# Kernel tuning notes

Measured on AMD Instinct MI355X. Metric: run time of the kernel, lower is better.

The kernel has to match this reference:

```python
import jax, jax.numpy as jnp
import numpy as np

B, S, D, H, F = 2, 2048, 1024, 16, 4096
DK = D // H
EPS = 1e-6


def _ln(x, g, b):
    mu = jnp.mean(x, axis=-1, keepdims=True)
    var = jnp.mean(jnp.square(x - mu), axis=-1, keepdims=True)
    return (x - mu) * jax.lax.rsqrt(var + EPS) * g + b


def setup_inputs() -> dict:
    key = jax.random.key(0)
    ks = jax.random.split(key, 8)
    sc = 0.02
    return {
        "x": jax.random.normal(ks[0], (B, S, D), jnp.float32),
        "wq": jax.random.normal(ks[1], (D, D), jnp.float32) * sc,
        "bq": jnp.zeros((D,), jnp.float32),
        "wk": jax.random.normal(ks[2], (D, D), jnp.float32) * sc,
        "bk": jnp.zeros((D,), jnp.float32),
        "wv": jax.random.normal(ks[3], (D, D), jnp.float32) * sc,
        "bv": jnp.zeros((D,), jnp.float32),
        "wo": jax.random.normal(ks[4], (D, D), jnp.float32) * sc,
        "bo": jnp.zeros((D,), jnp.float32),
        "w1": jax.random.normal(ks[5], (D, F), jnp.float32) * sc,
        "b1": jnp.zeros((F,), jnp.float32),
        "w2": jax.random.normal(ks[6], (F, D), jnp.float32) * sc,
        "b2": jnp.zeros((D,), jnp.float32),
        "g1": jnp.ones((D,), jnp.float32),
        "be1": jnp.zeros((D,), jnp.float32),
        "g2": jnp.ones((D,), jnp.float32),
        "be2": jnp.zeros((D,), jnp.float32),
    }


def reference(x, wq, bq, wk, bk, wv, bv, wo, bo, w1, b1, w2, b2, g1, be1, g2, be2):
    # Multi-head self-attention (no masks, eval-mode dropout = identity)
    q = (x @ wq + bq).reshape(B, S, H, DK)
    k = (x @ wk + bk).reshape(B, S, H, DK)
    v = (x @ wv + bv).reshape(B, S, H, DK)
    scale = 1.0 / (DK ** 0.5)
    score = jnp.einsum('bihd,bjhd->bhij', q, k) * scale  # [B,H,S,S]
    p = jax.nn.softmax(score, axis=-1)
    attn = jnp.einsum('bhij,bjhd->bihd', p, v).reshape(B, S, D)
    attn = attn @ wo + bo
    # residual + LayerNorm 1
    h = _ln(x + attn, g1, be1)
    # FFN (relu) + residual + LayerNorm 2
    ff = jax.nn.relu(h @ w1 + b1) @ w2 + b2
    return _ln(h + ff, g2, be2)
```

## Files before the change

### kernel.cpp

```cpp
#include <hip/hip_runtime.h>
#include <hip/hip_bf16.h>
#include <cmath>

typedef __bf16 bf16_t;
typedef __bf16 bf16x4 __attribute__((ext_vector_type(4)));
typedef __bf16 bf16x8 __attribute__((ext_vector_type(8)));
typedef float  f32x4  __attribute__((ext_vector_type(4)));

__device__ __forceinline__ void gld_lds16(const bf16_t* g, bf16_t* l) {
    __builtin_amdgcn_global_load_lds(
        (const __attribute__((address_space(1))) void*)g,
        (__attribute__((address_space(3))) void*)l,
        16, 0, 0);
}


struct PrepArgs {
    const float* w[6]; bf16_t* wt[6];
    int K[6], N[6], start[6];
    const float* x; bf16_t* xb; int castStart;
    const float* bq; const float* bk; float* bqkv; int biasStart;
};

__global__ __launch_bounds__(256) void prep(PrepArgs pa) {
    __shared__ float tile[32][33];
    const int bid = blockIdx.x, t = threadIdx.x;
    if (bid < pa.castStart) {
        int mi = 0;
#pragma unroll
        for (int i = 1; i < 6; i++) if (bid >= pa.start[i]) mi = i;
        const int tt  = bid - pa.start[mi];
        const int nbx = pa.N[mi] >> 5;
        const int n0 = (tt % nbx) * 32, k0 = (tt / nbx) * 32;
        const float* in = pa.w[mi];
        bf16_t* out = pa.wt[mi];
        const int K = pa.K[mi], N = pa.N[mi];
        const int tx = t & 31, ty = t >> 5;
#pragma unroll
        for (int i = 0; i < 4; i++) {
            int kk = ty + i * 8;
            tile[kk][tx] = in[(size_t)(k0 + kk) * N + n0 + tx];
        }
        __syncthreads();
#pragma unroll
        for (int i = 0; i < 4; i++) {
            int nn = ty + i * 8;
            out[(size_t)(n0 + nn) * K + k0 + tx] = (bf16_t)tile[tx][nn];
        }
    } else if (bid < pa.biasStart) {
        int i = (bid - pa.castStart) * 256 + t;
        f32x4 v = ((const f32x4*)pa.x)[i];
        bf16x4 o;
        o[0] = (bf16_t)v[0]; o[1] = (bf16_t)v[1]; o[2] = (bf16_t)v[2]; o[3] = (bf16_t)v[3];
        ((bf16x4*)pa.xb)[i] = o;
    } else {
#pragma unroll
        for (int j = 0; j < 8; j++) {
            int idx = t * 8 + j;
            pa.bqkv[idx] = idx < 1024 ? pa.bq[idx] : pa.bk[idx - 1024];
        }
    }
}

__global__ __launch_bounds__(512, 1) void gemm_deep(
    const bf16_t* __restrict__ A, const bf16_t* __restrict__ Bt,
    const float* __restrict__ bias, bf16_t* __restrict__ Cb,
    int N, int lda, int K, int relu, int nbn) {
    __shared__ __attribute__((aligned(16))) bf16_t As[4][256 * 32];
    __shared__ __attribute__((aligned(16))) bf16_t Bs[4][256 * 32];
    const int tid  = threadIdx.x;
    const int lane = tid & 63;
    const int wave = tid >> 6;
    const int wm = wave >> 2, wn = wave & 3;

    const int span  = 8 * nbn;
    const int group = blockIdx.x / span;
    const int rem   = blockIdx.x % span;
    const int bm    = group * 8 + (rem & 7);
    const int bn    = rem >> 3;

    const int srow   = tid >> 2;
    const int slot_s = ((tid & 3) ^ ((tid >> 3) & 3)) * 8;
    const bf16_t* Ag = A  + (size_t)(bm * 256 + srow) * lda + slot_s;
    const bf16_t* Bg = Bt + (size_t)(bn * 256 + srow) * lda + slot_s;

    auto stage = [&](int kk, int buf) {
        gld_lds16(Ag + kk,                       &As[buf][0]        + tid * 8);
        gld_lds16(Ag + (size_t)128 * lda + kk,   &As[buf][128 * 32] + tid * 8);
        gld_lds16(Bg + kk,                       &Bs[buf][0]        + tid * 8);
        gld_lds16(Bg + (size_t)128 * lda + kk,   &Bs[buf][128 * 32] + tid * 8);
    };

    f32x4 acc[8][4] = {};
    const int mrow = lane & 15;
    const int qsw  = (((lane >> 4) ^ ((mrow >> 1) & 3))) * 8;

    auto compute = [&](int cur) {
        bf16x8 bfr[4], af[8];
#pragma unroll
        for (int n = 0; n < 4; n++)
            bfr[n] = *(const bf16x8*)(&Bs[cur][(wn * 64 + n * 16 + mrow) * 32 + qsw]);
#pragma unroll
        for (int mt = 0; mt < 8; mt++)
            af[mt] = *(const bf16x8*)(&As[cur][(wm * 128 + mt * 16 + mrow) * 32 + qsw]);
        __builtin_amdgcn_s_setprio(1);
#pragma unroll
        for (int mt = 0; mt < 8; mt++)
#pragma unroll
            for (int n = 0; n < 4; n++)
                acc[mt][n] = __builtin_amdgcn_mfma_f32_16x16x32_bf16(
                    af[mt], bfr[n], acc[mt][n], 0, 0, 0);
        __builtin_amdgcn_s_setprio(0);
    };

    stage(0, 0); stage(32, 1); stage(64, 2);
    const int nst = K >> 5;
    for (int t = 0; t + 3 < nst; ++t) {
        stage((t + 3) * 32, (t + 3) & 3);
        asm volatile("s_waitcnt vmcnt(12)" ::: "memory");
        __builtin_amdgcn_s_barrier();
        compute(t & 3);
        asm volatile("s_waitcnt lgkmcnt(0)" ::: "memory");
        __builtin_amdgcn_s_barrier();
    }
    asm volatile("s_waitcnt vmcnt(8)" ::: "memory");
    __builtin_amdgcn_s_barrier();
    compute((nst - 3) & 3);
    asm volatile("s_waitcnt lgkmcnt(0)" ::: "memory");
    __builtin_amdgcn_s_barrier();
    asm volatile("s_waitcnt vmcnt(4)" ::: "memory");
    __builtin_amdgcn_s_barrier();
    compute((nst - 2) & 3);
    asm volatile("s_waitcnt lgkmcnt(0)" ::: "memory");
    __builtin_amdgcn_s_barrier();
    asm volatile("s_waitcnt vmcnt(0)" ::: "memory");
    __builtin_amdgcn_s_barrier();
    compute((nst - 1) & 3);

    const int rq = (lane >> 4) * 4;
#pragma unroll
    for (int mt = 0; mt < 8; mt++) {
        int row0 = bm * 256 + wm * 128 + mt * 16 + rq;
#pragma unroll
        for (int n = 0; n < 4; n++) {
            int col = bn * 256 + wn * 64 + n * 16 + mrow;
            float bvc = bias ? bias[col] : 0.f;
#pragma unroll
            for (int r = 0; r < 4; r++) {
                float v = acc[mt][n][r] + bvc;
                if (relu) v = fmaxf(v, 0.f);
                Cb[(size_t)(row0 + r) * N + col] = (bf16_t)v;
            }
        }
    }
}

template<int BN>
__global__ __launch_bounds__(512, 2) void gemm_bt256(
    const bf16_t* __restrict__ A, const bf16_t* __restrict__ Bt,
    const float* __restrict__ bias,
    float* __restrict__ Cf, bf16_t* __restrict__ Cb,
    int M, int N, int lda, int Kloc, int relu, int nbn,
    long bt_bstride, long c_bstride) {
    constexpr int NT = BN / 64;
    constexpr int WN = BN / 4;
    __shared__ __attribute__((aligned(16))) bf16_t As[2][2][256 * 32];
    __shared__ __attribute__((aligned(16))) bf16_t Bs[2][2][BN * 32];
    const int tid  = threadIdx.x;
    const int lane = tid & 63;
    const int wave = tid >> 6;
    const int wm = wave >> 2, wn = wave & 3;
    const int kh = blockIdx.z;

    const int span  = 8 * nbn;
    const int group = blockIdx.x / span;
    const int rem   = blockIdx.x % span;
    const int bm    = group * 8 + (rem & 7);
    const int bn    = rem >> 3;

    const bf16_t* Bt_b = Bt + (size_t)blockIdx.y * bt_bstride;
    float*  Cf_b = Cf ? Cf + (size_t)blockIdx.y * c_bstride + (size_t)kh * M * N : nullptr;
    bf16_t* Cb_b = Cb ? Cb + (size_t)blockIdx.y * c_bstride : nullptr;
    const int koff = kh * Kloc;

    const int r4 = tid >> 2;
    const int kcs = ((tid & 3) ^ ((tid >> 3) & 3)) * 8;
    const bf16_t* Ag = A    + (size_t)(bm * 256 + r4) * lda + koff + kcs;
    const bf16_t* Bg = Bt_b + (size_t)(bn * BN  + r4) * lda + koff + kcs;

    f32x4 acc[8][NT] = {};
    const int mrow = lane & 15;
    const int qsw  = (((lane >> 4) ^ ((mrow >> 1) & 3))) * 8;

    auto stage = [&](int kk, int buf) {
#pragma unroll
        for (int hh = 0; hh < 2; hh++) {
#pragma unroll
            for (int i = 0; i < 2; i++)
                gld_lds16(Ag + (size_t)(i * 128) * lda + kk + hh * 32,
                          &As[buf][hh][i * 128 * 32] + tid * 8);
            if (BN == 256) {
#pragma unroll
                for (int i = 0; i < 2; i++)
                    gld_lds16(Bg + (size_t)(i * 128) * lda + kk + hh * 32,
                              &Bs[buf][hh][i * 128 * 32] + tid * 8);
            } else {
                gld_lds16(Bg + kk + hh * 32, &Bs[buf][hh][0] + tid * 8);
            }
        }
    };

    stage(0, 0);
    __syncthreads();

    const int nsteps = Kloc >> 6;
    for (int st = 0; st < nsteps; ++st) {
        const int cur = st & 1;
        if (st + 1 < nsteps) stage((st + 1) << 6, cur ^ 1);

#pragma unroll
        for (int hh = 0; hh < 2; hh++) {
            bf16x8 bfr[NT];
#pragma unroll
            for (int n = 0; n < NT; n++)
                bfr[n] = *(const bf16x8*)(&Bs[cur][hh][(wn * WN + n * 16 + mrow) * 32 + qsw]);
#pragma unroll
            for (int mt = 0; mt < 8; mt++) {
                bf16x8 af = *(const bf16x8*)(&As[cur][hh][(wm * 128 + mt * 16 + mrow) * 32 + qsw]);
#pragma unroll
                for (int n = 0; n < NT; n++)
                    acc[mt][n] = __builtin_amdgcn_mfma_f32_16x16x32_bf16(
                        af, bfr[n], acc[mt][n], 0, 0, 0);
            }
        }
        __syncthreads();
    }

    const int rq = (lane >> 4) * 4;
#pragma unroll
    for (int mt = 0; mt < 8; mt++) {
        int row0 = bm * 256 + wm * 128 + mt * 16 + rq;
#pragma unroll
        for (int n = 0; n < NT; n++) {
            int col = bn * BN + wn * WN + n * 16 + mrow;
            float bvc = (bias && kh == 0) ? bias[col] : 0.f;
#pragma unroll
            for (int r = 0; r < 4; r++) {
                float v = acc[mt][n][r] + bvc;
                if (relu) v = fmaxf(v, 0.f);
                size_t idx = (size_t)(row0 + r) * N + col;
                if (Cf_b) Cf_b[idx] = v;
                if (Cb_b) Cb_b[idx] = (bf16_t)v;
            }
        }
    }
}

template<int MT>
__global__ __launch_bounds__(256) void gemm_bt(
    const bf16_t* __restrict__ A, const bf16_t* __restrict__ Bt,
    const float* __restrict__ bias,
    float* __restrict__ Cf, bf16_t* __restrict__ Cb,
    int M, int N, int lda, int Kloc, int relu, int nbn, int bias_row,
    long bt_bstride, long c_bstride) {
    constexpr int TM = MT * 32;
    __shared__ __attribute__((aligned(16))) bf16_t As[2][TM * 32];
    __shared__ __attribute__((aligned(16))) bf16_t Bs[2][128 * 32];
    const int tid  = threadIdx.x;
    const int lane = tid & 63;
    const int wave = tid >> 6;
    const int wm = wave & 1, wn = wave >> 1;
    const int kh = blockIdx.z;

    const int span  = 8 * nbn;
    const int group = blockIdx.x / span;
    const int rem   = blockIdx.x % span;
    const int bm    = group * 8 + (rem & 7);
    const int bn    = rem >> 3;

    const bf16_t* Bt_b = Bt + (size_t)blockIdx.y * bt_bstride;
    float*  Cf_b = Cf ? Cf + (size_t)blockIdx.y * c_bstride + (size_t)kh * M * N : nullptr;
    bf16_t* Cb_b = Cb ? Cb + (size_t)blockIdx.y * c_bstride : nullptr;
    const int koff = kh * Kloc;

    const int r4 = tid >> 2;
    const int kcs = ((tid & 3) ^ ((tid >> 3) & 3)) * 8;
    const bf16_t* Ag = A    + (size_t)(bm * TM  + r4) * lda + koff + kcs;
    const bf16_t* Bg = Bt_b + (size_t)(bn * 128 + r4) * lda + koff + kcs;

    f32x4 acc[MT][4] = {};
    const int mrow = lane & 15;
    const int qsw  = (((lane >> 4) ^ ((mrow >> 1) & 3))) * 8;

    auto stage = [&](int kk, int buf) {
#pragma unroll
        for (int i = 0; i < MT / 2; i++)
            gld_lds16(Ag + (size_t)(i * 64) * lda + kk, &As[buf][i * 64 * 32] + tid * 8);
        gld_lds16(Bg + kk,                        &Bs[buf][0] + tid * 8);
        gld_lds16(Bg + (size_t)64 * lda + kk,     &Bs[buf][64 * 32] + tid * 8);
    };

    stage(0, 0);
    __syncthreads();

    const int nt = Kloc >> 5;
    for (int t7 = 0; t7 < nt; ++t7) {
        const int cur = t7 & 1;
        if (t7 + 1 < nt) stage((t7 + 1) << 5, cur ^ 1);

        bf16x8 af[MT], bfr[4];
#pragma unroll
        for (int mt = 0; mt < MT; mt++)
            af[mt] = *(const bf16x8*)(&As[cur][(wm * (MT * 16) + mt * 16 + mrow) * 32 + qsw]);
#pragma unroll
        for (int nt2 = 0; nt2 < 4; nt2++)
            bfr[nt2] = *(const bf16x8*)(&Bs[cur][(wn * 64 + nt2 * 16 + mrow) * 32 + qsw]);
#pragma unroll
        for (int mt = 0; mt < MT; mt++)
#pragma unroll
            for (int nt2 = 0; nt2 < 4; nt2++)
                acc[mt][nt2] = __builtin_amdgcn_mfma_f32_16x16x32_bf16(
                    af[mt], bfr[nt2], acc[mt][nt2], 0, 0, 0);

        __syncthreads();
    }

    const int rq = (lane >> 4) * 4;
#pragma unroll
    for (int mt = 0; mt < MT; mt++) {
        int row0 = bm * TM + wm * (MT * 16) + mt * 16 + rq;
#pragma unroll
        for (int nt2 = 0; nt2 < 4; nt2++) {
            int col = bn * 128 + wn * 64 + nt2 * 16 + mrow;
            float bvc = (bias && kh == 0 && !bias_row) ? bias[col] : 0.f;
#pragma unroll
            for (int r = 0; r < 4; r++) {
                float bb = (bias && kh == 0 && bias_row) ? bias[row0 + r] : bvc;
                float v = acc[mt][nt2][r] + bb;
                if (relu) v = fmaxf(v, 0.f);
                size_t idx = (size_t)(row0 + r) * N + col;
                if (Cf_b) Cf_b[idx] = v;
                if (Cb_b) Cb_b[idx] = (bf16_t)v;
            }
        }
    }
}

__global__ __launch_bounds__(256) void flash_attn_mfma(
    const bf16_t* __restrict__ QKb,
    const bf16_t* __restrict__ Vtg,
    bf16_t* __restrict__ Outb) {
    __shared__ __attribute__((aligned(16))) bf16_t Ks[2][4096];
    __shared__ __attribute__((aligned(16))) bf16_t Vs[2][4096];
    __shared__ __attribute__((aligned(16))) bf16_t Ps[4096];
    const int t = threadIdx.x;
    const int lane = t & 63, wave = t >> 6;
    const int g = lane >> 4, cl = lane & 15;
    const int b = blockIdx.z, h = blockIdx.y, q0 = blockIdx.x * 64;
    const int RS = 2048;
    const bf16_t* Qg = QKb + (size_t)(b * 2048 + q0) * RS + h * 64;
    const bf16_t* Kg = QKb + (size_t)(b * 2048) * RS + 1024 + h * 64;
    const bf16_t* Vg = Vtg + ((size_t)b * 1024 + h * 64) * 2048;

    const int sr  = t >> 2;
    const int scs = (((t & 3) ^ ((t >> 3) & 3))) * 8;

    const bf16_t* Qrow = Qg + (size_t)(wave * 16 + cl) * RS;
    bf16x8 qr0 = *(const bf16x8*)(Qrow + g * 8);
    bf16x8 qr1 = *(const bf16x8*)(Qrow + 32 + g * 8);

    gld_lds16(Kg + (size_t)sr * RS + scs,        &Ks[0][0]    + t * 8);
    gld_lds16(Kg + (size_t)sr * RS + 32 + scs,   &Ks[0][2048] + t * 8);
    gld_lds16(Vg + (size_t)sr * 2048 + scs,      &Vs[0][0]    + t * 8);
    gld_lds16(Vg + (size_t)sr * 2048 + 32 + scs, &Vs[0][2048] + t * 8);
    __syncthreads();

    f32x4 Oacc[4] = {};
    f32x4 Lacc = {};
    bf16x8 ones;
#pragma unroll
    for (int j = 0; j < 8; j++) ones[j] = (bf16_t)1.0f;

    const int rowb = wave * 16 + cl;
    const int psw  = (cl & 7) << 4;
    const int gsw  = ((g ^ ((cl >> 1) & 3))) * 8;
    char* PsB = (char*)Ps;
    const float C = 0.125f * 1.4426950408889634f;

    for (int kt_i = 0; kt_i < 32; ++kt_i) {
        const int cur = kt_i & 1;
        if (kt_i + 1 < 32) {
            const int nb  = cur ^ 1;
            const int ktn = (kt_i + 1) * 64;
            gld_lds16(Kg + (size_t)(ktn + sr) * RS + scs,       &Ks[nb][0]    + t * 8);
            gld_lds16(Kg + (size_t)(ktn + sr) * RS + 32 + scs,  &Ks[nb][2048] + t * 8);
            gld_lds16(Vg + (size_t)sr * 2048 + ktn + scs,       &Vs[nb][0]    + t * 8);
            gld_lds16(Vg + (size_t)sr * 2048 + ktn + 32 + scs,  &Vs[nb][2048] + t * 8);
        }

        f32x4 Sacc[4] = {};
        __builtin_amdgcn_s_setprio(1);
#pragma unroll
        for (int ks = 0; ks < 2; ++ks) {
            bf16x8 bq = ks ? qr1 : qr0;
#pragma unroll
            for (int mt = 0; mt < 4; ++mt) {
                bf16x8 ak = *(const bf16x8*)(&Ks[cur][ks * 2048 + (mt * 16 + cl) * 32 + gsw]);
                Sacc[mt] = __builtin_amdgcn_mfma_f32_16x16x32_bf16(ak, bq, Sacc[mt], 0, 0, 0);
            }
        }
        __builtin_amdgcn_s_setprio(0);

#pragma unroll
        for (int mt = 0; mt < 4; ++mt) {
            bf16x4 p4;
#pragma unroll
            for (int r = 0; r < 4; r++)
                p4[r] = (bf16_t)__builtin_amdgcn_exp2f(Sacc[mt][r] * C);
            *(bf16x4*)(PsB + ((rowb * 128 + mt * 32 + g * 8) ^ psw)) = p4;
        }

        __builtin_amdgcn_s_setprio(1);
#pragma unroll
        for (int ks = 0; ks < 2; ++ks) {
            bf16x8 ap = *(const bf16x8*)(PsB + ((rowb * 128 + ks * 64 + g * 16) ^ psw));
            Lacc = __builtin_amdgcn_mfma_f32_16x16x32_bf16(ap, ones, Lacc, 0, 0, 0);
#pragma unroll
            for (int nt = 0; nt < 4; ++nt) {
                bf16x8 bv = *(const bf16x8*)(&Vs[cur][ks * 2048 + (nt * 16 + cl) * 32 + gsw]);
                Oacc[nt] = __builtin_amdgcn_mfma_f32_16x16x32_bf16(ap, bv, Oacc[nt], 0, 0, 0);
            }
        }
        __builtin_amdgcn_s_setprio(0);

        __syncthreads();
    }

#pragma unroll
    for (int r = 0; r < 4; r++) {
        float inv = 1.f / Lacc[r];
        int qrow = q0 + wave * 16 + g * 4 + r;
        size_t base = (size_t)(b * 2048 + qrow) * 1024 + h * 64;
#pragma unroll
        for (int nt = 0; nt < 4; nt++)
            Outb[base + nt * 16 + cl] = (bf16_t)(Oacc[nt][r] * inv);
    }
}

__global__ __launch_bounds__(256) void resid_ln3(const float* __restrict__ a,
                                                 const float* __restrict__ p0,
                                                 const float* __restrict__ p1,
                                                 const float* __restrict__ g,
                                                 const float* __restrict__ be,
                                                 float* __restrict__ outf,
                                                 bf16_t* __restrict__ outb) {
    const int row = blockIdx.x, t = threadIdx.x;
    const size_t base = (size_t)row * 1024;
    f32x4 v = ((const f32x4*)(a + base))[t] + ((const f32x4*)(p0 + base))[t];
    if (p1) v += ((const f32x4*)(p1 + base))[t];
    float sum = v[0] + v[1] + v[2] + v[3];
    float sq  = v[0] * v[0] + v[1] * v[1] + v[2] * v[2] + v[3] * v[3];
#pragma unroll
    for (int o = 1; o < 64; o <<= 1) {
        sum += __shfl_xor(sum, o);
        sq  += __shfl_xor(sq, o);
    }
    __shared__ float red[8];
    int wave = t >> 6, lane = t & 63;
    if (lane == 0) { red[wave] = sum; red[4 + wave] = sq; }
    __syncthreads();
    sum = red[0] + red[1] + red[2] + red[3];
    sq  = red[4] + red[5] + red[6] + red[7];
    float mu  = sum * (1.f / 1024.f);
    float var = sq * (1.f / 1024.f) - mu * mu;
    float rs  = rsqrtf(var + 1e-6f);
    f32x4 g4 = ((const f32x4*)g)[t];
    f32x4 b4 = ((const f32x4*)be)[t];
    f32x4 o = (v - mu) * rs * g4 + b4;
    ((f32x4*)(outf + base))[t] = o;
    if (outb) {
        bf16x4 ob;
        ob[0] = (bf16_t)o[0]; ob[1] = (bf16_t)o[1]; ob[2] = (bf16_t)o[2]; ob[3] = (bf16_t)o[3];
        ((bf16x4*)(outb + base))[t] = ob;
    }
}

extern "C" void kernel_launch(void* const* d_in, const int* in_sizes, int n_in,
                              void* d_out, int out_size, void* d_ws, size_t ws_size,
                              hipStream_t stream) {
    (void)in_sizes; (void)n_in; (void)out_size; (void)ws_size;
    const float* x   = (const float*)d_in[0];
    const float* wq  = (const float*)d_in[1];
    const float* bq  = (const float*)d_in[2];
    const float* wk  = (const float*)d_in[3];
    const float* bk  = (const float*)d_in[4];
    const float* wv  = (const float*)d_in[5];
    const float* bv  = (const float*)d_in[6];
    const float* wo  = (const float*)d_in[7];
    const float* bo  = (const float*)d_in[8];
    const float* w1  = (const float*)d_in[9];
    const float* b1  = (const float*)d_in[10];
    const float* w2  = (const float*)d_in[11];
    const float* b2  = (const float*)d_in[12];
    const float* g1  = (const float*)d_in[13];
    const float* be1 = (const float*)d_in[14];
    const float* g2  = (const float*)d_in[15];
    const float* be2 = (const float*)d_in[16];
    float* out = (float*)d_out;

    char* ws = (char*)d_ws;
    const size_t MB = 1ull << 20;
    bf16_t* xb    = (bf16_t*)(ws + 0);
    bf16_t* WtQKV = (bf16_t*)(ws + 8 * MB);
    bf16_t* WtO   = (bf16_t*)(ws + 14 * MB);
    bf16_t* Wt1   = (bf16_t*)(ws + 16 * MB);
    bf16_t* Wt2   = (bf16_t*)(ws + 24 * MB);
    float*  bqkv  = (float*)(ws + 32 * MB);
    bf16_t* QKb   = (bf16_t*)(ws + 33 * MB);
    bf16_t* Vt    = (bf16_t*)(ws + 49 * MB);
    bf16_t* ffb   = (bf16_t*)(ws + 33 * MB);
    float*  oa    = (float*)(ws + 65 * MB);
    float*  f2    = (float*)(ws + 65 * MB);
    float*  hbuf  = (float*)(ws + 97 * MB);
    bf16_t* hb    = (bf16_t*)(ws + 113 * MB);
    bf16_t* ab    = xb;
    const int MN = 4096 * 1024;

    PrepArgs pa;
    pa.w[0] = wq; pa.w[1] = wk; pa.w[2] = wv; pa.w[3] = wo; pa.w[4] = w1; pa.w[5] = w2;
    pa.wt[0] = WtQKV; pa.wt[1] = WtQKV + 1024 * 1024; pa.wt[2] = WtQKV + 2048 * 1024;
    pa.wt[3] = WtO; pa.wt[4] = Wt1; pa.wt[5] = Wt2;
    int Ks[6] = {1024, 1024, 1024, 1024, 1024, 4096};
    int Ns[6] = {1024, 1024, 1024, 1024, 4096, 1024};
    int st[6] = {0, 1024, 2048, 3072, 4096, 8192};
    for (int i = 0; i < 6; i++) { pa.K[i] = Ks[i]; pa.N[i] = Ns[i]; pa.start[i] = st[i]; }
    pa.x = x; pa.xb = xb; pa.castStart = 12288;
    pa.bq = bq; pa.bk = bk; pa.bqkv = bqkv; pa.biasStart = 12288 + 4096;
    prep<<<12288 + 4096 + 1, 256, 0, stream>>>(pa);

    gemm_bt256<128><<<256, 512, 0, stream>>>(xb, WtQKV, bqkv, nullptr, QKb,
                                        4096, 2048, 1024, 1024, 0, 16, 0, 0);
    gemm_bt<2><<<dim3(256, 2, 1), 256, 0, stream>>>(WtQKV + 2048 * 1024, xb, bv,
                                        nullptr, Vt, 1024, 2048, 1024, 1024, 0, 16, 1,
                                        (long)2048 * 1024, (long)1024 * 2048);
    flash_attn_mfma<<<dim3(32, 16, 2), 256, 0, stream>>>(QKb, Vt, ab);
    gemm_bt256<128><<<dim3(128, 1, 2), 512, 0, stream>>>(ab, WtO, bo, oa, nullptr,
                                        4096, 1024, 1024, 512, 0, 8, 0, 0);
    resid_ln3<<<4096, 256, 0, stream>>>(x, oa, oa + MN, g1, be1, hbuf, hb);
    gemm_deep<<<256, 512, 0, stream>>>(hb, Wt1, b1, ffb, 4096, 1024, 1024, 1, 16);
    gemm_bt256<128><<<dim3(128, 1, 2), 512, 0, stream>>>(ffb, Wt2, b2, f2, nullptr,
                                        4096, 1024, 4096, 2048, 0, 8, 0, 0);
    resid_ln3<<<4096, 256, 0, stream>>>(hbuf, f2, f2 + MN, g2, be2, out, nullptr);
}
```

Baseline: 390.2 us.

## Replace double-buffered GEMM with templated 4-stage deep pipeline; fold softmax scale into Q

Generalizes the 4-stage prefetch GEMM kernel to support a 128-wide N tile and split-K output, then uses it for the QK projection, output projection and FFN2 GEMMs in place of the 2-stage double-buffered kernel. The aim is to hide global-to-LDS latency behind more in-flight stages. Per-stage vmcnt waits are adjusted for the smaller B tile. The flash attention kernel also pre-multiplies Q by the softmax scale once, removing a multiply per score element. This adds a bf16 rounding of scaled Q. The deeper kernel uses launch_bounds(512,1) and more LDS, which may lower occupancy.

```diff
diff --git a/kernel.cpp b/kernel.cpp
--- a/kernel.cpp
+++ b/kernel.cpp
@@ -62,16 +62,21 @@
     }
 }
 
+template<int BN>
 __global__ __launch_bounds__(512, 1) void gemm_deep(
     const bf16_t* __restrict__ A, const bf16_t* __restrict__ Bt,
-    const float* __restrict__ bias, bf16_t* __restrict__ Cb,
-    int N, int lda, int K, int relu, int nbn) {
+    const float* __restrict__ bias,
+    float* __restrict__ Cf, bf16_t* __restrict__ Cb,
+    int M, int N, int lda, int Kloc, int relu, int nbn) {
+    constexpr int NT = BN / 64;
+    constexpr int WN = BN / 4;
     __shared__ __attribute__((aligned(16))) bf16_t As[4][256 * 32];
-    __shared__ __attribute__((aligned(16))) bf16_t Bs[4][256 * 32];
+    __shared__ __attribute__((aligned(16))) bf16_t Bs[4][BN * 32];
     const int tid  = threadIdx.x;
     const int lane = tid & 63;
     const int wave = tid >> 6;
     const int wm = wave >> 2, wn = wave & 3;
+    const int kh = blockIdx.z;
 
     const int span  = 8 * nbn;
     const int group = blockIdx.x / span;
@@ -79,27 +84,31 @@
     const int bm    = group * 8 + (rem & 7);
     const int bn    = rem >> 3;
 
+    float*  Cf_b = Cf ? Cf + (size_t)kh * M * N : nullptr;
+    const int koff = kh * Kloc;
+
     const int srow   = tid >> 2;
     const int slot_s = ((tid & 3) ^ ((tid >> 3) & 3)) * 8;
-    const bf16_t* Ag = A  + (size_t)(bm * 256 + srow) * lda + slot_s;
-    const bf16_t* Bg = Bt + (size_t)(bn * 256 + srow) * lda + slot_s;
+    const bf16_t* Ag = A  + (size_t)(bm * 256 + srow) * lda + koff + slot_s;
+    const bf16_t* Bg = Bt + (size_t)(bn * BN  + srow) * lda + koff + slot_s;
 
     auto stage = [&](int kk, int buf) {
         gld_lds16(Ag + kk,                       &As[buf][0]        + tid * 8);
         gld_lds16(Ag + (size_t)128 * lda + kk,   &As[buf][128 * 32] + tid * 8);
         gld_lds16(Bg + kk,                       &Bs[buf][0]        + tid * 8);
-        gld_lds16(Bg + (size_t)128 * lda + kk,   &Bs[buf][128 * 32] + tid * 8);
+        if constexpr (BN == 256)
+            gld_lds16(Bg + (size_t)128 * lda + kk, &Bs[buf][128 * 32] + tid * 8);
     };
 
-    f32x4 acc[8][4] = {};
+    f32x4 acc[8][NT] = {};
     const int mrow = lane & 15;
     const int qsw  = (((lane >> 4) ^ ((mrow >> 1) & 3))) * 8;
 
     auto compute = [&](int cur) {
-        bf16x8 bfr[4], af[8];
-#pragma unroll
-        for (int n = 0; n < 4; n++)
-            bfr[n] = *(const bf16x8*)(&Bs[cur][(wn * 64 + n * 16 + mrow) * 32 + qsw]);
+        bf16x8 bfr[NT], af[8];
+#pragma unroll
+        for (int n = 0; n < NT; n++)
+            bfr[n] = *(const bf16x8*)(&Bs[cur][(wn * WN + n * 16 + mrow) * 32 + qsw]);
 #pragma unroll
         for (int mt = 0; mt < 8; mt++)
             af[mt] = *(const bf16x8*)(&As[cur][(wm * 128 + mt * 16 + mrow) * 32 + qsw]);
@@ -107,28 +116,31 @@
 #pragma unroll
         for (int mt = 0; mt < 8; mt++)
 #pragma unroll
-            for (int n = 0; n < 4; n++)
+            for (int n = 0; n < NT; n++)
                 acc[mt][n] = __builtin_amdgcn_mfma_f32_16x16x32_bf16(
                     af[mt], bfr[n], acc[mt][n], 0, 0, 0);
         __builtin_amdgcn_s_setprio(0);
     };
 
     stage(0, 0); stage(32, 1); stage(64, 2);
-    const int nst = K >> 5;
+    const int nst = Kloc >> 5;
     for (int t = 0; t + 3 < nst; ++t) {
         stage((t + 3) * 32, (t + 3) & 3);
-        asm volatile("s_waitcnt vmcnt(12)" ::: "memory");
+        if constexpr (BN == 256) asm volatile("s_waitcnt vmcnt(12)" ::: "memory");
+        else                     asm volatile("s_waitcnt vmcnt(9)"  ::: "memory");
         __builtin_amdgcn_s_barrier();
         compute(t & 3);
         asm volatile("s_waitcnt lgkmcnt(0)" ::: "memory");
         __builtin_amdgcn_s_barrier();
     }
-    asm volatile("s_waitcnt vmcnt(8)" ::: "memory");
+    if constexpr (BN == 256) asm volatile("s_waitcnt vmcnt(8)" ::: "memory");
+    else                     asm volatile("s_waitcnt vmcnt(6)" ::: "memory");
     __builtin_amdgcn_s_barrier();
     compute((nst - 3) & 3);
     asm volatile("s_waitcnt lgkmcnt(0)" ::: "memory");
     __builtin_amdgcn_s_barrier();
-    asm volatile("s_waitcnt vmcnt(4)" ::: "memory");
+    if constexpr (BN == 256) asm volatile("s_waitcnt vmcnt(4)" ::: "memory");
+    else                     asm volatile("s_waitcnt vmcnt(3)" ::: "memory");
     __builtin_amdgcn_s_barrier();
     compute((nst - 2) & 3);
     asm volatile("s_waitcnt lgkmcnt(0)" ::: "memory");
@@ -142,105 +154,6 @@
     for (int mt = 0; mt < 8; mt++) {
         int row0 = bm * 256 + wm * 128 + mt * 16 + rq;
 #pragma unroll
-        for (int n = 0; n < 4; n++) {
-            int col = bn * 256 + wn * 64 + n * 16 + mrow;
-            float bvc = bias ? bias[col] : 0.f;
-#pragma unroll
-            for (int r = 0; r < 4; r++) {
-                float v = acc[mt][n][r] + bvc;
-                if (relu) v = fmaxf(v, 0.f);
-                Cb[(size_t)(row0 + r) * N + col] = (bf16_t)v;
-            }
-        }
-    }
-}
-
-template<int BN>
-__global__ __launch_bounds__(512, 2) void gemm_bt256(
-    const bf16_t* __restrict__ A, const bf16_t* __restrict__ Bt,
-    const float* __restrict__ bias,
-    float* __restrict__ Cf, bf16_t* __restrict__ Cb,
-    int M, int N, int lda, int Kloc, int relu, int nbn,
-    long bt_bstride, long c_bstride) {
-    constexpr int NT = BN / 64;
-    constexpr int WN = BN / 4;
-    __shared__ __attribute__((aligned(16))) bf16_t As[2][2][256 * 32];
-    __shared__ __attribute__((aligned(16))) bf16_t Bs[2][2][BN * 32];
-    const int tid  = threadIdx.x;
-    const int lane = tid & 63;
-    const int wave = tid >> 6;
-    const int wm = wave >> 2, wn = wave & 3;
-    const int kh = blockIdx.z;
-
-    const int span  = 8 * nbn;
-    const int group = blockIdx.x / span;
-    const int rem   = blockIdx.x % span;
-    const int bm    = group * 8 + (rem & 7);
-    const int bn    = rem >> 3;
-
-    const bf16_t* Bt_b = Bt + (size_t)blockIdx.y * bt_bstride;
-    float*  Cf_b = Cf ? Cf + (size_t)blockIdx.y * c_bstride + (size_t)kh * M * N : nullptr;
-    bf16_t* Cb_b = Cb ? Cb + (size_t)blockIdx.y * c_bstride : nullptr;
-    const int koff = kh * Kloc;
-
-    const int r4 = tid >> 2;
-    const int kcs = ((tid & 3) ^ ((tid >> 3) & 3)) * 8;
-    const bf16_t* Ag = A    + (size_t)(bm * 256 + r4) * lda + koff + kcs;
-    const bf16_t* Bg = Bt_b + (size_t)(bn * BN  + r4) * lda + koff + kcs;
-
-    f32x4 acc[8][NT] = {};
-    const int mrow = lane & 15;
-    const int qsw  = (((lane >> 4) ^ ((mrow >> 1) & 3))) * 8;
-
-    auto stage = [&](int kk, int buf) {
-#pragma unroll
-        for (int hh = 0; hh < 2; hh++) {
-#pragma unroll
-            for (int i = 0; i < 2; i++)
-                gld_lds16(Ag + (size_t)(i * 128) * lda + kk + hh * 32,
-                          &As[buf][hh][i * 128 * 32] + tid * 8);
-            if (BN == 256) {
-#pragma unroll
-                for (int i = 0; i < 2; i++)
-                    gld_lds16(Bg + (size_t)(i * 128) * lda + kk + hh * 32,
-                              &Bs[buf][hh][i * 128 * 32] + tid * 8);
-            } else {
-                gld_lds16(Bg + kk + hh * 32, &Bs[buf][hh][0] + tid * 8);
-            }
-        }
-    };
-
-    stage(0, 0);
-    __syncthreads();
-
-    const int nsteps = Kloc >> 6;
-    for (int st = 0; st < nsteps; ++st) {
-        const int cur = st & 1;
-        if (st + 1 < nsteps) stage((st + 1) << 6, cur ^ 1);
-
-#pragma unroll
-        for (int hh = 0; hh < 2; hh++) {
-            bf16x8 bfr[NT];
-#pragma unroll
-            for (int n = 0; n < NT; n++)
-                bfr[n] = *(const bf16x8*)(&Bs[cur][hh][(wn * WN + n * 16 + mrow) * 32 + qsw]);
-#pragma unroll
-            for (int mt = 0; mt < 8; mt++) {
-                bf16x8 af = *(const bf16x8*)(&As[cur][hh][(wm * 128 + mt * 16 + mrow) * 32 + qsw]);
-#pragma unroll
-                for (int n = 0; n < NT; n++)
-                    acc[mt][n] = __builtin_amdgcn_mfma_f32_16x16x32_bf16(
-                        af, bfr[n], acc[mt][n], 0, 0, 0);
-            }
-        }
-        __syncthreads();
-    }
-
-    const int rq = (lane >> 4) * 4;
-#pragma unroll
-    for (int mt = 0; mt < 8; mt++) {
-        int row0 = bm * 256 + wm * 128 + mt * 16 + rq;
-#pragma unroll
         for (int n = 0; n < NT; n++) {
             int col = bn * BN + wn * WN + n * 16 + mrow;
             float bvc = (bias && kh == 0) ? bias[col] : 0.f;
@@ -250,7 +163,7 @@
                 if (relu) v = fmaxf(v, 0.f);
                 size_t idx = (size_t)(row0 + r) * N + col;
                 if (Cf_b) Cf_b[idx] = v;
-                if (Cb_b) Cb_b[idx] = (bf16_t)v;
+                if (Cb)   Cb[idx]   = (bf16_t)v;
             }
         }
     }
@@ -365,9 +278,15 @@
     const int sr  = t >> 2;
     const int scs = (((t & 3) ^ ((t >> 3) & 3))) * 8;
 
+    const float C = 0.125f * 1.4426950408889634f;
     const bf16_t* Qrow = Qg + (size_t)(wave * 16 + cl) * RS;
     bf16x8 qr0 = *(const bf16x8*)(Qrow + g * 8);
     bf16x8 qr1 = *(const bf16x8*)(Qrow + 32 + g * 8);
+#pragma unroll
+    for (int j = 0; j < 8; j++) {
+        qr0[j] = (bf16_t)((float)qr0[j] * C);
+        qr1[j] = (bf16_t)((float)qr1[j] * C);
+    }
 
     gld_lds16(Kg + (size_t)sr * RS + scs,        &Ks[0][0]    + t * 8);
     gld_lds16(Kg + (size_t)sr * RS + 32 + scs,   &Ks[0][2048] + t * 8);
@@ -385,7 +304,6 @@
     const int psw  = (cl & 7) << 4;
     const int gsw  = ((g ^ ((cl >> 1) & 3))) * 8;
     char* PsB = (char*)Ps;
-    const float C = 0.125f * 1.4426950408889634f;
 
     for (int kt_i = 0; kt_i < 32; ++kt_i) {
         const int cur = kt_i & 1;
@@ -416,7 +334,7 @@
             bf16x4 p4;
 #pragma unroll
             for (int r = 0; r < 4; r++)
-                p4[r] = (bf16_t)__builtin_amdgcn_exp2f(Sacc[mt][r] * C);
+                p4[r] = (bf16_t)__builtin_amdgcn_exp2f(Sacc[mt][r]);
             *(bf16x4*)(PsB + ((rowb * 128 + mt * 32 + g * 8) ^ psw)) = p4;
         }
 
@@ -538,17 +456,18 @@
     pa.bq = bq; pa.bk = bk; pa.bqkv = bqkv; pa.biasStart = 12288 + 4096;
     prep<<<12288 + 4096 + 1, 256, 0, stream>>>(pa);
 
-    gemm_bt256<128><<<256, 512, 0, stream>>>(xb, WtQKV, bqkv, nullptr, QKb,
-                                        4096, 2048, 1024, 1024, 0, 16, 0, 0);
+    gemm_deep<128><<<256, 512, 0, stream>>>(xb, WtQKV, bqkv, nullptr, QKb,
+                                        4096, 2048, 1024, 1024, 0, 16);
     gemm_bt<2><<<dim3(256, 2, 1), 256, 0, stream>>>(WtQKV + 2048 * 1024, xb, bv,
                                         nullptr, Vt, 1024, 2048, 1024, 1024, 0, 16, 1,
                                         (long)2048 * 1024, (long)1024 * 2048);
     flash_attn_mfma<<<dim3(32, 16, 2), 256, 0, stream>>>(QKb, Vt, ab);
-    gemm_bt256<128><<<dim3(128, 1, 2), 512, 0, stream>>>(ab, WtO, bo, oa, nullptr,
-                                        4096, 1024, 1024, 512, 0, 8, 0, 0);
+    gemm_deep<128><<<dim3(128, 1, 2), 512, 0, stream>>>(ab, WtO, bo, oa, nullptr,
+                                        4096, 1024, 1024, 512, 0, 8);
     resid_ln3<<<4096, 256, 0, stream>>>(x, oa, oa + MN, g1, be1, hbuf, hb);
-    gemm_deep<<<256, 512, 0, stream>>>(hb, Wt1, b1, ffb, 4096, 1024, 1024, 1, 16);
-    gemm_bt256<128><<<dim3(128, 1, 2), 512, 0, stream>>>(ffb, Wt2, b2, f2, nullptr,
-                                        4096, 1024, 4096, 2048, 0, 8, 0, 0);
+    gemm_deep<256><<<256, 512, 0, stream>>>(hb, Wt1, b1, nullptr, ffb,
+                                        4096, 4096, 1024, 1024, 1, 16);
+    gemm_deep<128><<<dim3(128, 1, 2), 512, 0, stream>>>(ffb, Wt2, b2, f2, nullptr,
+                                        4096, 1024, 4096, 2048, 0, 8);
     resid_ln3<<<4096, 256, 0, stream>>>(hbuf, f2, f2 + MN, g2, be2, out, nullptr);
 }
```

Result: no change. 393.8 us (+0.9%).

## Widen flash-attention blocks to 128 queries and pre-scale Q; templatize deep GEMM

Applied to the files above, without the earlier changes.

The flash attention kernel now runs 512 threads per block and covers 128 query rows, so each staged K/V tile is shared by twice as many queries. Each thread issues one K and one V load per tile, with the half index picking the column. Q is multiplied by the softmax scale once at load time, which removes a multiply per score element. gemm_deep is templated on BN and gains split-K and an fp32 output path, but it is still launched with BN=256 and no split, and the extra P shared memory adds LDS pressure per block.

```diff
diff --git a/kernel.cpp b/kernel.cpp
--- a/kernel.cpp
+++ b/kernel.cpp
@@ -62,16 +62,21 @@
     }
 }
 
+template<int BN>
 __global__ __launch_bounds__(512, 1) void gemm_deep(
     const bf16_t* __restrict__ A, const bf16_t* __restrict__ Bt,
-    const float* __restrict__ bias, bf16_t* __restrict__ Cb,
-    int N, int lda, int K, int relu, int nbn) {
+    const float* __restrict__ bias,
+    float* __restrict__ Cf, bf16_t* __restrict__ Cb,
+    int M, int N, int lda, int Kloc, int relu, int nbn) {
+    constexpr int NT = BN / 64;
+    constexpr int WN = BN / 4;
     __shared__ __attribute__((aligned(16))) bf16_t As[4][256 * 32];
-    __shared__ __attribute__((aligned(16))) bf16_t Bs[4][256 * 32];
+    __shared__ __attribute__((aligned(16))) bf16_t Bs[4][BN * 32];
     const int tid  = threadIdx.x;
     const int lane = tid & 63;
     const int wave = tid >> 6;
     const int wm = wave >> 2, wn = wave & 3;
+    const int kh = blockIdx.z;
 
     const int span  = 8 * nbn;
     const int group = blockIdx.x / span;
@@ -79,27 +84,31 @@
     const int bm    = group * 8 + (rem & 7);
     const int bn    = rem >> 3;
 
+    float*  Cf_b = Cf ? Cf + (size_t)kh * M * N : nullptr;
+    const int koff = kh * Kloc;
+
     const int srow   = tid >> 2;
     const int slot_s = ((tid & 3) ^ ((tid >> 3) & 3)) * 8;
-    const bf16_t* Ag = A  + (size_t)(bm * 256 + srow) * lda + slot_s;
-    const bf16_t* Bg = Bt + (size_t)(bn * 256 + srow) * lda + slot_s;
+    const bf16_t* Ag = A  + (size_t)(bm * 256 + srow) * lda + koff + slot_s;
+    const bf16_t* Bg = Bt + (size_t)(bn * BN  + srow) * lda + koff + slot_s;
 
     auto stage = [&](int kk, int buf) {
         gld_lds16(Ag + kk,                       &As[buf][0]        + tid * 8);
         gld_lds16(Ag + (size_t)128 * lda + kk,   &As[buf][128 * 32] + tid * 8);
         gld_lds16(Bg + kk,                       &Bs[buf][0]        + tid * 8);
-        gld_lds16(Bg + (size_t)128 * lda + kk,   &Bs[buf][128 * 32] + tid * 8);
+        if constexpr (BN == 256)
+            gld_lds16(Bg + (size_t)128 * lda + kk, &Bs[buf][128 * 32] + tid * 8);
     };
 
-    f32x4 acc[8][4] = {};
+    f32x4 acc[8][NT] = {};
     const int mrow = lane & 15;
     const int qsw  = (((lane >> 4) ^ ((mrow >> 1) & 3))) * 8;
 
     auto compute = [&](int cur) {
-        bf16x8 bfr[4], af[8];
-#pragma unroll
-        for (int n = 0; n < 4; n++)
-            bfr[n] = *(const bf16x8*)(&Bs[cur][(wn * 64 + n * 16 + mrow) * 32 + qsw]);
+        bf16x8 bfr[NT], af[8];
+#pragma unroll
+        for (int n = 0; n < NT; n++)
+            bfr[n] = *(const bf16x8*)(&Bs[cur][(wn * WN + n * 16 + mrow) * 32 + qsw]);
 #pragma unroll
         for (int mt = 0; mt < 8; mt++)
             af[mt] = *(const bf16x8*)(&As[cur][(wm * 128 + mt * 16 + mrow) * 32 + qsw]);
@@ -107,28 +116,31 @@
 #pragma unroll
         for (int mt = 0; mt < 8; mt++)
 #pragma unroll
-            for (int n = 0; n < 4; n++)
+            for (int n = 0; n < NT; n++)
                 acc[mt][n] = __builtin_amdgcn_mfma_f32_16x16x32_bf16(
                     af[mt], bfr[n], acc[mt][n], 0, 0, 0);
         __builtin_amdgcn_s_setprio(0);
     };
 
     stage(0, 0); stage(32, 1); stage(64, 2);
-    const int nst = K >> 5;
+    const int nst = Kloc >> 5;
     for (int t = 0; t + 3 < nst; ++t) {
         stage((t + 3) * 32, (t + 3) & 3);
-        asm volatile("s_waitcnt vmcnt(12)" ::: "memory");
+        if constexpr (BN == 256) asm volatile("s_waitcnt vmcnt(12)" ::: "memory");
+        else                     asm volatile("s_waitcnt vmcnt(9)"  ::: "memory");
         __builtin_amdgcn_s_barrier();
         compute(t & 3);
         asm volatile("s_waitcnt lgkmcnt(0)" ::: "memory");
         __builtin_amdgcn_s_barrier();
     }
-    asm volatile("s_waitcnt vmcnt(8)" ::: "memory");
+    if constexpr (BN == 256) asm volatile("s_waitcnt vmcnt(8)" ::: "memory");
+    else                     asm volatile("s_waitcnt vmcnt(6)" ::: "memory");
     __builtin_amdgcn_s_barrier();
     compute((nst - 3) & 3);
     asm volatile("s_waitcnt lgkmcnt(0)" ::: "memory");
     __builtin_amdgcn_s_barrier();
-    asm volatile("s_waitcnt vmcnt(4)" ::: "memory");
+    if constexpr (BN == 256) asm volatile("s_waitcnt vmcnt(4)" ::: "memory");
+    else                     asm volatile("s_waitcnt vmcnt(3)" ::: "memory");
     __builtin_amdgcn_s_barrier();
     compute((nst - 2) & 3);
     asm volatile("s_waitcnt lgkmcnt(0)" ::: "memory");
@@ -142,14 +154,16 @@
     for (int mt = 0; mt < 8; mt++) {
         int row0 = bm * 256 + wm * 128 + mt * 16 + rq;
 #pragma unroll
-        for (int n = 0; n < 4; n++) {
-            int col = bn * 256 + wn * 64 + n * 16 + mrow;
-            float bvc = bias ? bias[col] : 0.f;
+        for (int n = 0; n < NT; n++) {
+            int col = bn * BN + wn * WN + n * 16 + mrow;
+            float bvc = (bias && kh == 0) ? bias[col] : 0.f;
 #pragma unroll
             for (int r = 0; r < 4; r++) {
                 float v = acc[mt][n][r] + bvc;
                 if (relu) v = fmaxf(v, 0.f);
-                Cb[(size_t)(row0 + r) * N + col] = (bf16_t)v;
+                size_t idx = (size_t)(row0 + r) * N + col;
+                if (Cf_b) Cf_b[idx] = v;
+                if (Cb)   Cb[idx]   = (bf16_t)v;
             }
         }
     }
@@ -346,33 +360,41 @@
     }
 }
 
-__global__ __launch_bounds__(256) void flash_attn_mfma(
+__global__ __launch_bounds__(512) void flash_attn_mfma(
     const bf16_t* __restrict__ QKb,
     const bf16_t* __restrict__ Vtg,
     bf16_t* __restrict__ Outb) {
     __shared__ __attribute__((aligned(16))) bf16_t Ks[2][4096];
     __shared__ __attribute__((aligned(16))) bf16_t Vs[2][4096];
-    __shared__ __attribute__((aligned(16))) bf16_t Ps[4096];
+    __shared__ __attribute__((aligned(16))) bf16_t Ps[8192];
     const int t = threadIdx.x;
     const int lane = t & 63, wave = t >> 6;
     const int g = lane >> 4, cl = lane & 15;
-    const int b = blockIdx.z, h = blockIdx.y, q0 = blockIdx.x * 64;
+    const int b = blockIdx.z, h = blockIdx.y, q0 = blockIdx.x * 128;
     const int RS = 2048;
     const bf16_t* Qg = QKb + (size_t)(b * 2048 + q0) * RS + h * 64;
     const bf16_t* Kg = QKb + (size_t)(b * 2048) * RS + 1024 + h * 64;
     const bf16_t* Vg = Vtg + ((size_t)b * 1024 + h * 64) * 2048;
 
-    const int sr  = t >> 2;
-    const int scs = (((t & 3) ^ ((t >> 3) & 3))) * 8;
-
+    const int sr   = (t >> 2) & 63;
+    const int half = t >> 8;
+    const int scs  = half * 32 + (((t & 3) ^ ((t >> 3) & 3)) * 8);
+
+    const float C = 0.125f * 1.4426950408889634f;
     const bf16_t* Qrow = Qg + (size_t)(wave * 16 + cl) * RS;
     bf16x8 qr0 = *(const bf16x8*)(Qrow + g * 8);
     bf16x8 qr1 = *(const bf16x8*)(Qrow + 32 + g * 8);
-
-    gld_lds16(Kg + (size_t)sr * RS + scs,        &Ks[0][0]    + t * 8);
-    gld_lds16(Kg + (size_t)sr * RS + 32 + scs,   &Ks[0][2048] + t * 8);
-    gld_lds16(Vg + (size_t)sr * 2048 + scs,      &Vs[0][0]    + t * 8);
-    gld_lds16(Vg + (size_t)sr * 2048 + 32 + scs, &Vs[0][2048] + t * 8);
+#pragma unroll
+    for (int j = 0; j < 8; j++) {
+        qr0[j] = (bf16_t)((float)qr0[j] * C);
+        qr1[j] = (bf16_t)((float)qr1[j] * C);
+    }
+
+    const bf16_t* Kst = Kg + (size_t)sr * RS + scs;
+    const bf16_t* Vst = Vg + (size_t)sr * 2048 + scs;
+
+    gld_lds16(Kst, &Ks[0][0] + t * 8);
+    gld_lds16(Vst, &Vs[0][0] + t * 8);
     __syncthreads();
 
     f32x4 Oacc[4] = {};
@@ -385,17 +407,14 @@
     const int psw  = (cl & 7) << 4;
     const int gsw  = ((g ^ ((cl >> 1) & 3))) * 8;
     char* PsB = (char*)Ps;
-    const float C = 0.125f * 1.4426950408889634f;
 
     for (int kt_i = 0; kt_i < 32; ++kt_i) {
         const int cur = kt_i & 1;
         if (kt_i + 1 < 32) {
-            const int nb  = cur ^ 1;
-            const int ktn = (kt_i + 1) * 64;
-            gld_lds16(Kg + (size_t)(ktn + sr) * RS + scs,       &Ks[nb][0]    + t * 8);
-            gld_lds16(Kg + (size_t)(ktn + sr) * RS + 32 + scs,  &Ks[nb][2048] + t * 8);
-            gld_lds16(Vg + (size_t)sr * 2048 + ktn + scs,       &Vs[nb][0]    + t * 8);
-            gld_lds16(Vg + (size_t)sr * 2048 + ktn + 32 + scs,  &Vs[nb][2048] + t * 8);
+            Kst += (size_t)64 * RS;
+            Vst += 64;
+            gld_lds16(Kst, &Ks[cur ^ 1][0] + t * 8);
+            gld_lds16(Vst, &Vs[cur ^ 1][0] + t * 8);
         }
 
         f32x4 Sacc[4] = {};
@@ -416,7 +435,7 @@
             bf16x4 p4;
 #pragma unroll
             for (int r = 0; r < 4; r++)
-                p4[r] = (bf16_t)__builtin_amdgcn_exp2f(Sacc[mt][r] * C);
+                p4[r] = (bf16_t)__builtin_amdgcn_exp2f(Sacc[mt][r]);
             *(bf16x4*)(PsB + ((rowb * 128 + mt * 32 + g * 8) ^ psw)) = p4;
         }
 
@@ -543,11 +562,12 @@
     gemm_bt<2><<<dim3(256, 2, 1), 256, 0, stream>>>(WtQKV + 2048 * 1024, xb, bv,
                                         nullptr, Vt, 1024, 2048, 1024, 1024, 0, 16, 1,
                                         (long)2048 * 1024, (long)1024 * 2048);
-    flash_attn_mfma<<<dim3(32, 16, 2), 256, 0, stream>>>(QKb, Vt, ab);
+    flash_attn_mfma<<<dim3(16, 16, 2), 512, 0, stream>>>(QKb, Vt, ab);
     gemm_bt256<128><<<dim3(128, 1, 2), 512, 0, stream>>>(ab, WtO, bo, oa, nullptr,
                                         4096, 1024, 1024, 512, 0, 8, 0, 0);
     resid_ln3<<<4096, 256, 0, stream>>>(x, oa, oa + MN, g1, be1, hbuf, hb);
-    gemm_deep<<<256, 512, 0, stream>>>(hb, Wt1, b1, ffb, 4096, 1024, 1024, 1, 16);
+    gemm_deep<256><<<256, 512, 0, stream>>>(hb, Wt1, b1, nullptr, ffb,
+                                        4096, 4096, 1024, 1024, 1, 16);
     gemm_bt256<128><<<dim3(128, 1, 2), 512, 0, stream>>>(ffb, Wt2, b2, f2, nullptr,
                                         4096, 1024, 4096, 2048, 0, 8, 0, 0);
     resid_ln3<<<4096, 256, 0, stream>>>(hbuf, f2, f2 + MN, g2, be2, out, nullptr);
```

Measured after the change: 381.9 us. 2.1% less time.
